# Performance work log

Hardware: AMD Instinct MI355X
Metric: run time of the kernel (lower is better)

## Reference

```python
import jax, jax.numpy as jnp
import numpy as np

NC = 80          # num classes (len(yolov8.names))
CONF = 0.25      # ultralytics conf_thres default
IOU_T = 0.45     # ultralytics iou_thres default
MAX_DET = 300    # module default max_det
K = 1024         # pre-NMS candidate cap (static stand-in for max_nms)
MAX_WH = 7680.0  # ultralytics class-offset for multi-class NMS


def setup_inputs() -> dict:
    key = jax.random.key(0)
    k1, k2, k3 = jax.random.split(key, 3)
    B, A = 32, 8400
    # YOLOv8 head layout: rows 0:4 = xywh (pixels), rows 4: = sigmoid class scores
    xy = jax.random.uniform(k1, (B, 2, A), dtype=jnp.float32) * 640.0
    wh = jax.random.uniform(k2, (B, 2, A), dtype=jnp.float32) * 160.0 + 8.0
    scores = jax.random.uniform(k3, (B, NC, A), dtype=jnp.float32) ** 3  # mostly below conf_thres
    preds = jnp.concatenate([xy, wh, scores], axis=1)  # [B, 4+NC, A]
    return {"preds": preds}


def _box_iou(b):
    # b: [K, 4] xyxy -> [K, K] pairwise IoU
    area = (b[:, 2] - b[:, 0]) * (b[:, 3] - b[:, 1])
    lt = jnp.maximum(b[:, None, :2], b[None, :, :2])
    rb = jnp.minimum(b[:, None, 2:], b[None, :, 2:])
    wh = jnp.clip(rb - lt, 0.0)
    inter = wh[..., 0] * wh[..., 1]
    return inter / (area[:, None] + area[None, :] - inter + 1e-7)


def _nms_single(pred):
    # pred: [4+NC, A]
    boxes_xywh = pred[:4].T           # [A, 4]
    cls_scores = pred[4:].T           # [A, NC]
    conf = cls_scores.max(-1)         # best-class confidence per anchor
    cls = jnp.argmax(cls_scores, -1)
    score = jnp.where(conf > CONF, conf, 0.0)
    top, idx = jax.lax.top_k(score, K)            # K candidates by confidence
    xywh = boxes_xywh[idx]
    half = xywh[:, 2:] * 0.5
    boxes = jnp.concatenate([xywh[:, :2] - half, xywh[:, :2] + half], -1)  # xyxy
    cls_k = cls[idx]
    valid = top > CONF
    # multi-class NMS via per-class coordinate offset (ultralytics trick)
    iou = _box_iou(boxes + (cls_k.astype(boxes.dtype) * MAX_WH)[:, None])
    ar = jnp.arange(K)

    def body(i, st):
        supp, keep = st
        ki = valid[i] & ~supp[i]
        keep = keep.at[i].set(ki)
        supp = supp | (ki & (iou[i] > IOU_T) & (ar > i))
        return supp, keep

    _, keep = jax.lax.fori_loop(0, K, body,
                                (jnp.zeros(K, bool), jnp.zeros(K, bool)))
    fscore = jnp.where(keep, top, 0.0)
    sc, order = jax.lax.top_k(fscore, MAX_DET)
    det = jnp.concatenate(
        [boxes[order], top[order][:, None], cls_k[order].astype(boxes.dtype)[:, None]], -1)
    # pad invalid rows with value NC in every column (matches F.pad(value=len(names)))
    return jnp.where((sc > CONF)[:, None], det, jnp.float32(NC))


def reference(preds):
    # [B, MAX_DET, 6] -> (x1, y1, x2, y2, conf, cls), padded rows filled with NC
    return jax.vmap(_nms_single)(preds)
```

## Files before the change

### kernel.cpp

```cpp
#include <hip/hip_runtime.h>
#include <stdint.h>

typedef unsigned long long u64;
typedef unsigned int u32;

#define NC 80
#define CONF_T 0.25f
#define IOU_THR 0.45f
#define MAX_DET 300
#define KBIG 1024
#define A_ANCH 8400
#define NROWS 84
#define MAX_WH 7680.0f
#define HBINS 256
#define BIN_BASE 0x3e80u

__global__ __launch_bounds__(512) void yolo_conf_kernel(const float* __restrict__ preds,
                                                        u64* __restrict__ keys) {
    int b = blockIdx.x / 9;
    int g = (blockIdx.x % 9) * 512 + threadIdx.x;
    if (g >= A_ANCH / 2) return;
    int a0 = g * 2;
    const float* base = preds + ((size_t)b * NROWS + 4) * A_ANCH + a0;
    float2 best = *(const float2*)base;
    int bc0 = 0, bc1 = 0;
#pragma unroll 8
    for (int c = 1; c < NC; ++c) {
        float2 v = *(const float2*)(base + (size_t)c * A_ANCH);
        if (v.x > best.x) { best.x = v.x; bc0 = c; }
        if (v.y > best.y) { best.y = v.y; bc1 = c; }
    }
    float s0 = (best.x > CONF_T) ? best.x : 0.0f;
    float s1 = (best.y > CONF_T) ? best.y : 0.0f;
    ulonglong2 kk;
    kk.x = ((u64)__float_as_uint(s0) << 32) | ((u64)(16383 - a0) << 7) | (u64)bc0;
    kk.y = ((u64)__float_as_uint(s1) << 32) | ((u64)(16383 - (a0 + 1)) << 7) | (u64)bc1;
    *(ulonglong2*)(keys + (size_t)b * A_ANCH + a0) = kk;
}

__device__ __forceinline__ float iou_f(float ix1, float iy1, float ix2, float iy2, float iar,
                                       float jx1, float jy1, float jx2, float jy2, float jar) {
    float lx = fmaxf(ix1, jx1), ly = fmaxf(iy1, jy1);
    float rx = fminf(ix2, jx2), ry = fminf(iy2, jy2);
    float ww = fmaxf(__fsub_rn(rx, lx), 0.0f);
    float hh = fmaxf(__fsub_rn(ry, ly), 0.0f);
    float inter = __fmul_rn(ww, hh);
    float den = __fadd_rn(__fsub_rn(__fadd_rn(iar, jar), inter), 1e-7f);
    return __fdiv_rn(inter, den);
}

__device__ __forceinline__ void hadd(u32* h, u32 bin, bool m, int lane) {
    u64 act = __ballot(m);
    if (act == 0) return;
    int fl = __ffsll((unsigned long long)act) - 1;
    u32 fb = __shfl(bin, fl);
    u64 same = __ballot(m && (bin == fb));
    if (lane == fl) atomicAdd(&h[fb], (u32)__popcll(same));
    if (m && (bin != fb)) atomicAdd(&h[bin], 1u);
}

__device__ __forceinline__ u64 bstep(u64 v, u32 idx, u32 size, u32 stride) {
    u64 v2 = __shfl_xor((unsigned long long)v, (int)stride, 64);
    bool keep_big = (((idx & stride) == 0) == ((idx & size) == 0));
    return ((v > v2) == keep_big) ? v : v2;
}

__device__ __forceinline__ void radix_scan(u32* hist, int nb, int shift, u32* s_scal,
                                           u32* wsum, int tid, int lane, int wid) {
    int per = nb >> 10; if (per == 0) per = 1;
    int na = nb / per;
    u32 rem = s_scal[1];
    u32 Pk = s_scal[0];
    int hi = nb - 1 - per * tid;
    u32 s = 0;
    if (tid < na)
        for (int q = 0; q < per; ++q) s += hist[hi - q];
    u32 pre = s;
#pragma unroll
    for (int off = 1; off < 64; off <<= 1) {
        u32 o = __shfl_up(pre, off);
        if (lane >= off) pre += o;
    }
    if (lane == 63) wsum[wid] = pre;
    __syncthreads();
    u32 base = 0;
    for (int w = 0; w < wid; ++w) base += wsum[w];
    u32 run = base + pre - s;
    if (tid < na) {
        for (int q = 0; q < per; ++q) {
            int d = hi - q;
            u32 g = hist[d];
            if (run < rem && rem <= run + g) {
                s_scal[0] = Pk | ((u32)d << shift);
                s_scal[1] = rem - run;
            }
            run += g;
        }
    }
    __syncthreads();
}

union U2 {
    u32 hist[4096];
    struct { u32 eqw[264]; u32 wpre[264]; } tie;
};

__global__ __launch_bounds__(1024) void yolo_nms_kernel(const float* __restrict__ preds,
                                                        const u64* __restrict__ keys,
                                                        float* __restrict__ out) {
    const int b = blockIdx.x;
    const int tid = threadIdx.x;
    const int lane = tid & 63;
    const int wid = tid >> 6;

    __shared__ U2 u2;
    __shared__ u64 skey[KBIG];
    __shared__ float BX1[KBIG], BY1[KBIG], BX2[KBIG], BY2[KBIG], BAR[KBIG];
    __shared__ int keptlist[364];
    __shared__ float kx1[364], ky1[364], kx2[364], ky2[364], kar[364];
    __shared__ u32 kcls[364];
    __shared__ u64 rows[64];
    __shared__ u32 wsum[16];
    __shared__ u32 s_scal[4];
    __shared__ u32 s_cnt;
    __shared__ u32 s_csupp[2];
    __shared__ u32 s_nkept;

    const u64* kb = keys + (size_t)b * A_ANCH;

    u32 vals[9];
#pragma unroll
    for (int it = 0; it < 9; ++it) {
        int a = tid + it * 1024;
        vals[it] = (a < A_ANCH) ? (u32)(kb[a] >> 32) : 0u;
    }

    if (tid < HBINS) u2.hist[tid] = 0;
    __syncthreads();
#pragma unroll
    for (int it = 0; it < 9; ++it) {
        int a = tid + it * 1024;
        u32 v = vals[it];
        u32 bin = (v >> 16) - BIN_BASE;
        if (bin > 255u) bin = 255u;
        hadd(u2.hist, bin, (a < A_ANCH) && (v != 0u), lane);
    }
    __syncthreads();

    {
        u32 g = (tid < HBINS) ? u2.hist[HBINS - 1 - tid] : 0u;
        u32 pre = g;
#pragma unroll
        for (int off = 1; off < 64; off <<= 1) {
            u32 o = __shfl_up(pre, off);
            if (lane >= off) pre += o;
        }
        if (lane == 63) wsum[wid] = pre;
        __syncthreads();
        u32 base = 0;
        for (int w = 0; w < wid; ++w) base += wsum[w];
        pre += base;
        u32 run = pre - g;
        if (tid < HBINS) {
            if (run < 512u && 512u <= pre) { s_scal[0] = (u32)(HBINS - 1 - tid); s_scal[2] = pre; }
            if (tid == HBINS - 1) {
                s_scal[3] = pre;
                if (pre < 512u) { s_scal[0] = 0; s_scal[2] = pre; }
            }
        }
        __syncthreads();
    }
    const u32 Pbin16 = BIN_BASE + s_scal[0];
    const u32 Cfast = s_scal[2];
    const u32 validN = s_scal[3];

    for (int pass = 0; pass < 2; ++pass) {
        u32 Ccand;
        if (pass == 0) {
            if (Cfast > (u32)KBIG) continue;
            Ccand = Cfast;
            skey[tid] = 0;
            if (tid == 0) { s_cnt = 0; s_nkept = 0; s_csupp[0] = 0; s_csupp[1] = 0; }
            __syncthreads();
#pragma unroll
            for (int it = 0; it < 9; ++it) {
                int a = tid + it * 1024;
                u32 v = vals[it];
                bool take = (a < A_ANCH) && (v != 0u) && ((v >> 16) >= Pbin16);
                u64 m = __ballot(take);
                if (m) {
                    int fl = __ffsll((unsigned long long)m) - 1;
                    u32 basep = 0;
                    if (lane == fl) basep = atomicAdd(&s_cnt, (u32)__popcll(m));
                    basep = __shfl(basep, fl);
                    if (take) {
                        u32 pos = basep + (u32)__popcll(m & ((1ull << lane) - 1ull));
                        if (pos < (u32)KBIG) skey[pos] = kb[a];
                    }
                }
            }
            __syncthreads();
        } else {
            for (int i = tid; i < 4096; i += 1024) u2.hist[i] = 0;
            if (tid == 0) {
                s_scal[0] = 0; s_scal[1] = (u32)KBIG; s_scal[2] = 0;
                s_nkept = 0; s_csupp[0] = 0; s_csupp[1] = 0;
            }
            __syncthreads();
#pragma unroll
            for (int it = 0; it < 9; ++it) {
                int a = tid + it * 1024;
                hadd(u2.hist, vals[it] >> 20, a < A_ANCH, lane);
            }
            __syncthreads();
            radix_scan(u2.hist, 4096, 20, s_scal, wsum, tid, lane, wid);
            for (int i = tid; i < 4096; i += 1024) u2.hist[i] = 0;
            __syncthreads();
            u32 Pk = s_scal[0];
#pragma unroll
            for (int it = 0; it < 9; ++it) {
                int a = tid + it * 1024;
                u32 v = vals[it];
                bool m = (a < A_ANCH) && ((v & 0xFFF00000u) == Pk);
                hadd(u2.hist, (v >> 8) & 4095u, m, lane);
            }
            __syncthreads();
            radix_scan(u2.hist, 4096, 8, s_scal, wsum, tid, lane, wid);
            for (int i = tid; i < 256; i += 1024) u2.hist[i] = 0;
            __syncthreads();
            Pk = s_scal[0];
#pragma unroll
            for (int it = 0; it < 9; ++it) {
                int a = tid + it * 1024;
                u32 v = vals[it];
                bool m = (a < A_ANCH) && ((v & 0xFFFFFF00u) == Pk);
                hadd(u2.hist, v & 255u, m, lane);
            }
            __syncthreads();
            radix_scan(u2.hist, 256, 0, s_scal, wsum, tid, lane, wid);
            const u32 P = s_scal[0];
            const u32 tEq = s_scal[1];
            if (tid < 264) u2.tie.eqw[tid] = 0;
            __syncthreads();
#pragma unroll
            for (int it = 0; it < 9; ++it) {
                int a = tid + it * 1024;
                if (a < A_ANCH && vals[it] == P) atomicOr(&u2.tie.eqw[a >> 5], 1u << (a & 31));
            }
            __syncthreads();
            if (wid == 0) {
                u32 cw[5], loc = 0;
#pragma unroll
                for (int q = 0; q < 5; ++q) {
                    int w2 = lane * 5 + q;
                    u32 e = (w2 < 264) ? u2.tie.eqw[w2] : 0u;
                    cw[q] = (u32)__popc(e); loc += cw[q];
                }
                u32 pre = loc;
#pragma unroll
                for (int off = 1; off < 64; off <<= 1) {
                    u32 o = __shfl_up(pre, off);
                    if (lane >= off) pre += o;
                }
                u32 run = pre - loc;
#pragma unroll
                for (int q = 0; q < 5; ++q) {
                    int w2 = lane * 5 + q;
                    if (w2 < 264) u2.tie.wpre[w2] = run;
                    run += cw[q];
                }
            }
            __syncthreads();
#pragma unroll
            for (int it = 0; it < 9; ++it) {
                int a = tid + it * 1024;
                bool take = false;
                if (a < A_ANCH) {
                    u32 v = vals[it];
                    take = v > P;
                    if (!take && v == P) {
                        u32 r = u2.tie.wpre[a >> 5] +
                                (u32)__popc(u2.tie.eqw[a >> 5] & ((1u << (a & 31)) - 1u));
                        take = (r < tEq);
                    }
                }
                u64 m = __ballot(take);
                if (m) {
                    int fl = __ffsll((unsigned long long)m) - 1;
                    u32 basep = 0;
                    if (lane == fl) basep = atomicAdd(&s_scal[2], (u32)__popcll(m));
                    basep = __shfl(basep, fl);
                    if (take) {
                        u32 pos = basep + (u32)__popcll(m & ((1ull << lane) - 1ull));
                        if (pos < (u32)KBIG) skey[pos] = kb[a];
                    }
                }
            }
            __syncthreads();
            Ccand = KBIG;
        }

        {
            u64 v = skey[tid];
#pragma unroll
            for (u32 size = 2; size <= 64; size <<= 1)
#pragma unroll
                for (u32 stride = size >> 1; stride >= 1; stride >>= 1)
                    v = bstep(v, (u32)tid, size, stride);
            for (u32 size = 128; size <= 1024; size <<= 1) {
                for (u32 stride = size >> 1; stride >= 64; stride >>= 1) {
                    skey[tid] = v;
                    __syncthreads();
                    u64 v2 = skey[tid ^ stride];
                    bool keep_big = ((((u32)tid & stride) == 0) == (((u32)tid & size) == 0));
                    v = ((v > v2) == keep_big) ? v : v2;
                    __syncthreads();
                }
#pragma unroll
                for (u32 stride = 32; stride >= 1; stride >>= 1)
                    v = bstep(v, (u32)tid, size, stride);
            }
            skey[tid] = v;
            __syncthreads();
        }

        {
            u64 key = skey[tid];
            int cls = (int)(key & 127u);
            int idx = 16383 - (int)((key >> 7) & 16383u);
            if (idx >= A_ANCH || idx < 0) idx = 0;
            const float* pb = preds + (size_t)b * NROWS * A_ANCH + idx;
            float x = pb[0];
            float y = pb[A_ANCH];
            float w = pb[2 * A_ANCH];
            float h = pb[3 * A_ANCH];
            float hw = __fmul_rn(w, 0.5f), hh = __fmul_rn(h, 0.5f);
            float x1 = __fsub_rn(x, hw), x2 = __fadd_rn(x, hw);
            float y1 = __fsub_rn(y, hh), y2 = __fadd_rn(y, hh);
            float off = __fmul_rn((float)cls, MAX_WH);
            float bx1 = __fadd_rn(x1, off), bx2 = __fadd_rn(x2, off);
            float by1 = __fadd_rn(y1, off), by2 = __fadd_rn(y2, off);
            BX1[tid] = bx1; BY1[tid] = by1; BX2[tid] = bx2; BY2[tid] = by2;
            BAR[tid] = __fmul_rn(__fsub_rn(bx2, bx1), __fsub_rn(by2, by1));
        }
        __syncthreads();

        const int nchunks = (int)((Ccand + 63u) >> 6);
        for (int c = 0; c < nchunks; ++c) {
            int j = c * 64 + lane;
            u64 keyj = skey[j];
            float scj = __uint_as_float((u32)(keyj >> 32));
            u32 clsj = (u32)(keyj & 127u);
            float jx1 = BX1[j], jy1 = BY1[j], jx2 = BX2[j], jy2 = BY2[j], jar = BAR[j];

            u32 nk = s_nkept;
            bool suppbit = false;
            for (u32 k = wid; k < nk; k += 16) {
                bool cm = (kcls[k] == clsj);
                if (__ballot(cm)) {
                    float iou = iou_f(kx1[k], ky1[k], kx2[k], ky2[k], kar[k],
                                      jx1, jy1, jx2, jy2, jar);
                    suppbit |= (cm && (iou > IOU_THR));
                }
            }
            u64 bm = __ballot(suppbit);
            if (bm && lane == 0) {
                atomicOr(&s_csupp[0], (u32)bm);
                atomicOr(&s_csupp[1], (u32)(bm >> 32));
            }
#pragma unroll
            for (int p2 = 0; p2 < 4; ++p2) {
                int i = p2 * 16 + wid;
                int ci = c * 64 + i;
                u32 clsi = (u32)(skey[ci] & 127u);
                u64 m = 0;
                if (__ballot(clsi == clsj)) {
                    float iou = iou_f(BX1[ci], BY1[ci], BX2[ci], BY2[ci], BAR[ci],
                                      jx1, jy1, jx2, jy2, jar);
                    m = __ballot((lane > i) && (iou > IOU_THR));
                }
                if (lane == 0) rows[i] = m;
            }
            __syncthreads();
            if (wid == 0) {
                u64 row = rows[lane];
                u32 rlo = (u32)row, rhi = (u32)(row >> 32);
                u64 csupp = (((u64)s_csupp[1]) << 32) | (u64)s_csupp[0];
                u64 validm = __ballot(scj > CONF_T) & ~csupp;
                u64 supp = 0, keep = 0;
#pragma unroll
                for (int i = 0; i < 64; ++i) {
                    u64 ri = (((u64)(u32)__builtin_amdgcn_readlane((int)rhi, i)) << 32) |
                             (u64)(u32)__builtin_amdgcn_readlane((int)rlo, i);
                    bool ki = (((validm & ~supp) >> i) & 1ull) != 0;
                    if (ki) { keep |= (1ull << i); supp |= ri; }
                }
                u32 basek = s_nkept;
                if ((keep >> lane) & 1ull) {
                    u32 slot = basek + (u32)__popcll(keep & ((1ull << lane) - 1ull));
                    keptlist[slot] = j;
                    kx1[slot] = jx1; ky1[slot] = jy1;
                    kx2[slot] = jx2; ky2[slot] = jy2;
                    kar[slot] = jar; kcls[slot] = clsj;
                }
                if (lane == 0) {
                    s_nkept = basek + (u32)__popcll(keep);
                    s_csupp[0] = 0; s_csupp[1] = 0;
                }
            }
            __syncthreads();
            if (s_nkept >= MAX_DET) break;
        }

        u32 nk = s_nkept;
        bool finished = (nk >= MAX_DET) || (Ccand >= validN) || (pass == 1);
        if (!finished) continue;

        if (tid < MAX_DET) {
            float row[6];
            int t = (tid < (int)(nk < MAX_DET ? nk : MAX_DET)) ? keptlist[tid] : -1;
            if (t >= 0) {
                u64 key = skey[t];
                float score = __uint_as_float((u32)(key >> 32));
                int cls = (int)(key & 127u);
                int idx = 16383 - (int)((key >> 7) & 16383u);
                const float* pb = preds + (size_t)b * NROWS * A_ANCH + idx;
                float x = pb[0], y = pb[A_ANCH], w = pb[2 * A_ANCH], h = pb[3 * A_ANCH];
                float hw = __fmul_rn(w, 0.5f), hh = __fmul_rn(h, 0.5f);
                row[0] = __fsub_rn(x, hw);
                row[1] = __fsub_rn(y, hh);
                row[2] = __fadd_rn(x, hw);
                row[3] = __fadd_rn(y, hh);
                row[4] = score;
                row[5] = (float)cls;
            } else {
                row[0] = row[1] = row[2] = row[3] = row[4] = row[5] = (float)NC;
            }
            float* o = out + ((size_t)b * MAX_DET + tid) * 6;
#pragma unroll
            for (int q = 0; q < 6; ++q) o[q] = row[q];
        }
        break;
    }
}

extern "C" void kernel_launch(void* const* d_in, const int* in_sizes, int n_in,
                              void* d_out, int out_size, void* d_ws, size_t ws_size,
                              hipStream_t stream) {
    const float* preds = (const float*)d_in[0];
    float* out = (float*)d_out;
    u64* keys = (u64*)d_ws;
    int B = in_sizes[0] / (NROWS * A_ANCH);
    yolo_conf_kernel<<<dim3(B * 9), dim3(512), 0, stream>>>(preds, keys);
    yolo_nms_kernel<<<dim3(B), dim3(1024), 0, stream>>>(preds, keys, out);
}
```

Measured before the change: 68.28 us.

## Move histogram and box decoding into a wide prep kernel before NMS

Adds a third kernel, launched with many blocks, that decodes xyxy boxes (both plain and class-offset) for every anchor into workspace and builds the per-image score histogram through shared-memory and global atomics. The single-block-per-image NMS kernel then reads the precomputed histogram and float4 boxes instead of building the histogram itself and gathering four strided columns per candidate. The goal is to shift serial work out of the 32-block NMS kernel, which leaves most of the GPU idle, onto a well-parallel kernel. In exchange it adds a kernel launch and extra global writes and reads of the box buffers. The histogram is zeroed in the conf kernel, so the new kernel depends on stream ordering.

```diff
diff --git a/kernel.cpp b/kernel.cpp
--- a/kernel.cpp
+++ b/kernel.cpp
@@ -15,10 +15,23 @@
 #define HBINS 256
 #define BIN_BASE 0x3e80u
 
+__device__ __forceinline__ void hadd(u32* h, u32 bin, bool m, int lane) {
+    u64 act = __ballot(m);
+    if (act == 0) return;
+    int fl = __ffsll((unsigned long long)act) - 1;
+    u32 fb = __shfl(bin, fl);
+    u64 same = __ballot(m && (bin == fb));
+    if (lane == fl) atomicAdd(&h[fb], (u32)__popcll(same));
+    if (m && (bin != fb)) atomicAdd(&h[bin], 1u);
+}
+
 __global__ __launch_bounds__(512) void yolo_conf_kernel(const float* __restrict__ preds,
-                                                        u64* __restrict__ keys) {
+                                                        u64* __restrict__ keys,
+                                                        u32* __restrict__ hist) {
     int b = blockIdx.x / 9;
-    int g = (blockIdx.x % 9) * 512 + threadIdx.x;
+    int slab = blockIdx.x % 9;
+    if (slab == 0 && threadIdx.x < HBINS) hist[(size_t)b * HBINS + threadIdx.x] = 0;
+    int g = slab * 512 + threadIdx.x;
     if (g >= A_ANCH / 2) return;
     int a0 = g * 2;
     const float* base = preds + ((size_t)b * NROWS + 4) * A_ANCH + a0;
@@ -38,6 +51,48 @@
     *(ulonglong2*)(keys + (size_t)b * A_ANCH + a0) = kk;
 }
 
+__global__ __launch_bounds__(256) void yolo_prep_kernel(const float* __restrict__ preds,
+                                                        const u64* __restrict__ keys,
+                                                        float4* __restrict__ obox,
+                                                        float4* __restrict__ pbox,
+                                                        u32* __restrict__ hist) {
+    __shared__ u32 lh[HBINS];
+    const int lane = threadIdx.x & 63;
+    int b = blockIdx.x / 33;
+    int a = (blockIdx.x % 33) * 256 + threadIdx.x;
+    lh[threadIdx.x] = 0;
+    __syncthreads();
+
+    u32 bits = 0, bin = 0;
+    bool act = a < A_ANCH;
+    if (act) {
+        u64 key = keys[(size_t)b * A_ANCH + a];
+        bits = (u32)(key >> 32);
+        int cls = (int)(key & 127u);
+        const float* pb = preds + (size_t)b * NROWS * A_ANCH + a;
+        float x = pb[0];
+        float y = pb[A_ANCH];
+        float w = pb[2 * A_ANCH];
+        float h = pb[3 * A_ANCH];
+        float hw = __fmul_rn(w, 0.5f), hh = __fmul_rn(h, 0.5f);
+        float x1 = __fsub_rn(x, hw), x2 = __fadd_rn(x, hw);
+        float y1 = __fsub_rn(y, hh), y2 = __fadd_rn(y, hh);
+        float4 pB; pB.x = x1; pB.y = y1; pB.z = x2; pB.w = y2;
+        pbox[(size_t)b * A_ANCH + a] = pB;
+        float off = __fmul_rn((float)cls, MAX_WH);
+        float4 oB;
+        oB.x = __fadd_rn(x1, off); oB.y = __fadd_rn(y1, off);
+        oB.z = __fadd_rn(x2, off); oB.w = __fadd_rn(y2, off);
+        obox[(size_t)b * A_ANCH + a] = oB;
+        bin = (bits >> 16) - BIN_BASE;
+        if (bin > 255u) bin = 255u;
+    }
+    hadd(lh, bin, act && (bits != 0u), lane);
+    __syncthreads();
+    u32 c = lh[threadIdx.x];
+    if (c) atomicAdd(&hist[(size_t)b * HBINS + threadIdx.x], c);
+}
+
 __device__ __forceinline__ float iou_f(float ix1, float iy1, float ix2, float iy2, float iar,
                                        float jx1, float jy1, float jx2, float jy2, float jar) {
     float lx = fmaxf(ix1, jx1), ly = fmaxf(iy1, jy1);
@@ -47,16 +102,6 @@
     float inter = __fmul_rn(ww, hh);
     float den = __fadd_rn(__fsub_rn(__fadd_rn(iar, jar), inter), 1e-7f);
     return __fdiv_rn(inter, den);
-}
-
-__device__ __forceinline__ void hadd(u32* h, u32 bin, bool m, int lane) {
-    u64 act = __ballot(m);
-    if (act == 0) return;
-    int fl = __ffsll((unsigned long long)act) - 1;
-    u32 fb = __shfl(bin, fl);
-    u64 same = __ballot(m && (bin == fb));
-    if (lane == fl) atomicAdd(&h[fb], (u32)__popcll(same));
-    if (m && (bin != fb)) atomicAdd(&h[bin], 1u);
 }
 
 __device__ __forceinline__ u64 bstep(u64 v, u32 idx, u32 size, u32 stride) {
@@ -105,8 +150,10 @@
     struct { u32 eqw[264]; u32 wpre[264]; } tie;
 };
 
-__global__ __launch_bounds__(1024) void yolo_nms_kernel(const float* __restrict__ preds,
-                                                        const u64* __restrict__ keys,
+__global__ __launch_bounds__(1024) void yolo_nms_kernel(const u64* __restrict__ keys,
+                                                        const float4* __restrict__ obox,
+                                                        const float4* __restrict__ pbox,
+                                                        const u32* __restrict__ hist,
                                                         float* __restrict__ out) {
     const int b = blockIdx.x;
     const int tid = threadIdx.x;
@@ -135,20 +182,9 @@
         vals[it] = (a < A_ANCH) ? (u32)(kb[a] >> 32) : 0u;
     }
 
-    if (tid < HBINS) u2.hist[tid] = 0;
-    __syncthreads();
-#pragma unroll
-    for (int it = 0; it < 9; ++it) {
-        int a = tid + it * 1024;
-        u32 v = vals[it];
-        u32 bin = (v >> 16) - BIN_BASE;
-        if (bin > 255u) bin = 255u;
-        hadd(u2.hist, bin, (a < A_ANCH) && (v != 0u), lane);
-    }
-    __syncthreads();
-
+    const u32* hb = hist + (size_t)b * HBINS;
     {
-        u32 g = (tid < HBINS) ? u2.hist[HBINS - 1 - tid] : 0u;
+        u32 g = (tid < HBINS) ? hb[HBINS - 1 - tid] : 0u;
         u32 pre = g;
 #pragma unroll
         for (int off = 1; off < 64; off <<= 1) {
@@ -326,22 +362,11 @@
 
         {
             u64 key = skey[tid];
-            int cls = (int)(key & 127u);
             int idx = 16383 - (int)((key >> 7) & 16383u);
             if (idx >= A_ANCH || idx < 0) idx = 0;
-            const float* pb = preds + (size_t)b * NROWS * A_ANCH + idx;
-            float x = pb[0];
-            float y = pb[A_ANCH];
-            float w = pb[2 * A_ANCH];
-            float h = pb[3 * A_ANCH];
-            float hw = __fmul_rn(w, 0.5f), hh = __fmul_rn(h, 0.5f);
-            float x1 = __fsub_rn(x, hw), x2 = __fadd_rn(x, hw);
-            float y1 = __fsub_rn(y, hh), y2 = __fadd_rn(y, hh);
-            float off = __fmul_rn((float)cls, MAX_WH);
-            float bx1 = __fadd_rn(x1, off), bx2 = __fadd_rn(x2, off);
-            float by1 = __fadd_rn(y1, off), by2 = __fadd_rn(y2, off);
-            BX1[tid] = bx1; BY1[tid] = by1; BX2[tid] = bx2; BY2[tid] = by2;
-            BAR[tid] = __fmul_rn(__fsub_rn(bx2, bx1), __fsub_rn(by2, by1));
+            float4 ob = obox[(size_t)b * A_ANCH + idx];
+            BX1[tid] = ob.x; BY1[tid] = ob.y; BX2[tid] = ob.z; BY2[tid] = ob.w;
+            BAR[tid] = __fmul_rn(__fsub_rn(ob.z, ob.x), __fsub_rn(ob.w, ob.y));
         }
         __syncthreads();
 
@@ -424,13 +449,9 @@
                 float score = __uint_as_float((u32)(key >> 32));
                 int cls = (int)(key & 127u);
                 int idx = 16383 - (int)((key >> 7) & 16383u);
-                const float* pb = preds + (size_t)b * NROWS * A_ANCH + idx;
-                float x = pb[0], y = pb[A_ANCH], w = pb[2 * A_ANCH], h = pb[3 * A_ANCH];
-                float hw = __fmul_rn(w, 0.5f), hh = __fmul_rn(h, 0.5f);
-                row[0] = __fsub_rn(x, hw);
-                row[1] = __fsub_rn(y, hh);
-                row[2] = __fadd_rn(x, hw);
-                row[3] = __fadd_rn(y, hh);
+                if (idx >= A_ANCH || idx < 0) idx = 0;
+                float4 pB = pbox[(size_t)b * A_ANCH + idx];
+                row[0] = pB.x; row[1] = pB.y; row[2] = pB.z; row[3] = pB.w;
                 row[4] = score;
                 row[5] = (float)cls;
             } else {
@@ -449,8 +470,12 @@
                               hipStream_t stream) {
     const float* preds = (const float*)d_in[0];
     float* out = (float*)d_out;
+    int B = in_sizes[0] / (NROWS * A_ANCH);
     u64* keys = (u64*)d_ws;
-    int B = in_sizes[0] / (NROWS * A_ANCH);
-    yolo_conf_kernel<<<dim3(B * 9), dim3(512), 0, stream>>>(preds, keys);
-    yolo_nms_kernel<<<dim3(B), dim3(1024), 0, stream>>>(preds, keys, out);
-}
+    float4* obox = (float4*)(keys + (size_t)B * A_ANCH);
+    float4* pbox = obox + (size_t)B * A_ANCH;
+    u32* hist = (u32*)(pbox + (size_t)B * A_ANCH);
+    yolo_conf_kernel<<<dim3(B * 9), dim3(512), 0, stream>>>(preds, keys, hist);
+    yolo_prep_kernel<<<dim3(B * 33), dim3(256), 0, stream>>>(preds, keys, obox, pbox, hist);
+    yolo_nms_kernel<<<dim3(B), dim3(1024), 0, stream>>>(keys, obox, pbox, hist, out);
+}
```

Measured after the change: 69.16 us. Within noise of the previous version (+1.3%).
